# Performance work log

Measured on AMD Instinct MI355X. Metric: run time of the kernel, lower is better.

## Reference

```python
import jax, jax.numpy as jnp
import numpy as np

VOCAB, VEC, HID, ATT, DOM, B, S = 50000, 300, 256, 500, 16, 64, 128


def _gru_scan(gi_all, h0, Whh, bhh):
    # gi_all: [S,B,3H] precomputed input projections; returns hs: [S,B,H]
    def step(h, gi):
        gh = h @ Whh.T + bhh
        i_r, i_z, i_n = jnp.split(gi, 3, axis=-1)
        h_r, h_z, h_n = jnp.split(gh, 3, axis=-1)
        r = jax.nn.sigmoid(i_r + h_r)
        zg = jax.nn.sigmoid(i_z + h_z)
        n = jnp.tanh(i_n + r * h_n)
        h_new = (1.0 - zg) * n + zg * h
        return h_new, h_new
    _, hs = jax.lax.scan(step, h0, gi_all)
    return hs


def setup_inputs() -> dict:
    key = jax.random.key(0)
    ks = jax.random.split(key, 16)
    def xavier(k, shape):
        fan_in, fan_out = shape[-1], shape[0]
        std = float(np.sqrt(2.0 / (fan_in + fan_out)))
        return jax.random.normal(k, shape, dtype=jnp.float32) * std
    inp = {
        'x': jax.random.randint(ks[0], (B, S), 0, VOCAB),
        'z': jax.random.randint(ks[1], (B,), 0, DOM),
        'emb': jax.random.normal(ks[2], (VOCAB, VEC), dtype=jnp.float32) * 0.1,
        'Wih_f': xavier(ks[3], (3 * HID, VEC)),
        'Whh_f': xavier(ks[4], (3 * HID, HID)),
        'bih_f': jnp.zeros((3 * HID,), jnp.float32),
        'bhh_f': jnp.zeros((3 * HID,), jnp.float32),
        'Wih_b': xavier(ks[5], (3 * HID, VEC)),
        'Whh_b': xavier(ks[6], (3 * HID, HID)),
        'bih_b': jnp.zeros((3 * HID,), jnp.float32),
        'bhh_b': jnp.zeros((3 * HID,), jnp.float32),
        'att_fc_W': xavier(ks[7], (ATT, 2 * HID)),
        'att_fc_b': jnp.zeros((ATT,), jnp.float32),
        'att_weight': xavier(ks[8], (DOM, ATT)),
        'fc_W': xavier(ks[9], (2, 2 * HID)),
        'fc_b': jnp.zeros((2,), jnp.float32),
    }
    return inp


def reference(x, z, emb, Wih_f, Whh_f, bih_f, bhh_f, Wih_b, Whh_b, bih_b, bhh_b,
              att_fc_W, att_fc_b, att_weight, fc_W, fc_b):
    xe = emb[x]                              # [B,S,VEC]
    xs = jnp.transpose(xe, (1, 0, 2))        # [S,B,VEC] (seq-major like torch GRU)
    h0 = jnp.zeros((x.shape[0], HID), jnp.float32)
    gi_f = jnp.einsum('sbv,gv->sbg', xs, Wih_f) + bih_f
    hs_f = _gru_scan(gi_f, h0, Whh_f, bhh_f)                       # [S,B,H]
    gi_b = jnp.einsum('sbv,gv->sbg', xs[::-1], Wih_b) + bih_b
    hs_b = _gru_scan(gi_b, h0, Whh_b, bhh_b)[::-1]                 # [S,B,H]
    h = jnp.transpose(jnp.concatenate([hs_f, hs_b], axis=-1), (1, 0, 2))  # [B,S,2H]
    hr = jnp.tanh(jnp.einsum('bsh,ah->bsa', h, att_fc_W) + att_fc_b)      # [B,S,ATT]
    # batched gather of per-domain attention vector, then per-row dot
    u = jnp.einsum('bsa,ba->bs', hr, att_weight[z])                        # [B,S]
    att = jax.nn.softmax(u, axis=1)                                        # [B,S]
    pooled = jnp.einsum('bsh,bs->bh', h, att)                              # [B,2H]
    # dropout is identity in eval mode
    return pooled @ fc_W.T + fc_b                                          # [B,2]
```

## Files before the change

kernel.cpp:

```cpp
#include <hip/hip_runtime.h>
#include <math.h>

#define VEC   300
#define HID   256
#define ATT   500
#define NB    64
#define NS    128
#define G3    768
#define GIC   1536
#define H2    512

typedef _Float16 half1;
typedef _Float16 h2_t  __attribute__((ext_vector_type(2)));
typedef _Float16 f16x8 __attribute__((ext_vector_type(8)));
typedef float    f32x4 __attribute__((ext_vector_type(4)));

struct __align__(16) H8 { h2_t a, b, c, d; };

#if __has_builtin(__builtin_amdgcn_exp2f)
#define EXP2F(x) __builtin_amdgcn_exp2f(x)
#else
#define EXP2F(x) exp2f(x)
#endif
#if __has_builtin(__builtin_amdgcn_rcpf)
#define RCPF(x) __builtin_amdgcn_rcpf(x)
#else
#define RCPF(x) (1.0f/(x))
#endif

__device__ __forceinline__ float sigm(float x){ return RCPF(1.f + EXP2F(-1.44269504f*x)); }
__device__ __forceinline__ float tanh_fast(float x){ return 1.f - 2.f*RCPF(1.f + EXP2F(2.88539008f*x)); }

#if __has_builtin(__builtin_amdgcn_fdot2)
#define FDOT(w,h,acc) __builtin_amdgcn_fdot2((w),(h),(acc),false)
#else
#define FDOT(w,h,acc) ((acc) + (float)(w).x*(float)(h).x + (float)(w).y*(float)(h).y)
#endif

__global__ __launch_bounds__(256) void k_prep2(const float* __restrict__ Wf,
                       const float* __restrict__ Wb, h2_t* __restrict__ Wpk){
  int o = blockIdx.x*256 + threadIdx.x;
  int t = o & 511;
  int rest = o >> 9;
  int j = rest % 3;
  int p = (rest/3) & 63;
  int dir = rest / 192;
  int u = (t >> 6)*32 + (t & 31);
  int ks = (t >> 5) & 1;
  const float* W = dir ? Wb : Wf;
  int k0 = ks*128 + 2*p;
  h2_t w;
  w.x = (half1)W[(j*HID+u)*HID + k0];
  w.y = (half1)W[(j*HID+u)*HID + k0 + 1];
  Wpk[o] = w;
}

__global__ __launch_bounds__(256) void k_prepA(const float* __restrict__ afW,
                       half1* __restrict__ afW16){
  int o = blockIdx.x*256 + threadIdx.x;
  int n = o >> 9, k = o & 511;
  afW16[o] = (half1)((n < ATT) ? afW[n*H2 + k] : 0.f);
}

__global__ __launch_bounds__(256)
__attribute__((amdgpu_waves_per_eu(4, 4)))
void k_gi_mfma(const int* __restrict__ x,
      const float* __restrict__ emb,
      const float* __restrict__ Wf, const float* __restrict__ Wb,
      const float* __restrict__ bf, const float* __restrict__ bb,
      float* __restrict__ gi){
  __shared__ half1 Al[128*40];
  __shared__ half1 Bl[128*40];
  __shared__ int   xi[128];
  const int t = threadIdx.x;
  const int row0 = blockIdx.x * 128;
  const int col0 = blockIdx.y * 128;
  if (t < 128) {
    int i = row0 + t; int s = i >> 6; int b = i & 63;
    xi[t] = x[b*NS + s];
  }
  __syncthreads();

  const int lane = t & 63, wid = t >> 6;
  const int wr = wid >> 1, wc = wid & 1;
  const int l15 = lane & 15, lk = lane >> 4;

  f32x4 acc[4][4];
#pragma unroll
  for (int i = 0; i < 4; ++i)
#pragma unroll
    for (int j = 0; j < 4; ++j) acc[i][j] = (f32x4){0.f,0.f,0.f,0.f};

  for (int ks = 0; ks < 10; ++ks) {
#pragma unroll
    for (int l = 0; l < 8; ++l) {
      int idx = l*256 + t;
      int row = idx >> 4;
      int kp  = idx & 15;
      int kk  = ks*32 + kp*2;
      h2_t va; va.x = (half1)0.f; va.y = (half1)0.f;
      h2_t vb; vb.x = (half1)0.f; vb.y = (half1)0.f;
      if (kk < VEC) {
        float2 e = *reinterpret_cast<const float2*>(&emb[(long)xi[row]*VEC + kk]);
        va.x = (half1)e.x; va.y = (half1)e.y;
        int g = col0 + row;
        const float* W = (g < G3) ? &Wf[(long)g*VEC] : &Wb[(long)(g-G3)*VEC];
        float2 w2 = *reinterpret_cast<const float2*>(&W[kk]);
        vb.x = (half1)w2.x; vb.y = (half1)w2.y;
      }
      *reinterpret_cast<h2_t*>(&Al[row*40 + kp*2]) = va;
      *reinterpret_cast<h2_t*>(&Bl[row*40 + kp*2]) = vb;
    }
    __syncthreads();
    f16x8 af[4], bfq[4];
#pragma unroll
    for (int i = 0; i < 4; ++i)
      af[i]  = *reinterpret_cast<const f16x8*>(&Al[(wr*64 + i*16 + l15)*40 + lk*8]);
#pragma unroll
    for (int j = 0; j < 4; ++j)
      bfq[j] = *reinterpret_cast<const f16x8*>(&Bl[(wc*64 + j*16 + l15)*40 + lk*8]);
#pragma unroll
    for (int i = 0; i < 4; ++i)
#pragma unroll
      for (int j = 0; j < 4; ++j)
        acc[i][j] = __builtin_amdgcn_mfma_f32_16x16x32_f16(af[i], bfq[j], acc[i][j], 0, 0, 0);
    __syncthreads();
  }

#pragma unroll
  for (int j = 0; j < 4; ++j) {
    int gcol = col0 + wc*64 + j*16 + l15;
    float bj = (gcol < G3) ? bf[gcol] : bb[gcol - G3];
#pragma unroll
    for (int i = 0; i < 4; ++i) {
      int grow0 = row0 + wr*64 + i*16 + lk*4;
#pragma unroll
      for (int q = 0; q < 4; ++q)
        gi[(long)(grow0 + q)*GIC + gcol] = acc[i][j][q] + bj;
    }
  }
}

#define DECL12(X,g,UNUSED) h2_t X##g##a0,X##g##a1,X##g##a2, X##g##b0,X##g##b1,X##g##b2, \
                                X##g##c0,X##g##c1,X##g##c2, X##g##d0,X##g##d1,X##g##d2;
#define LOAD12(X,g,PB) \
  X##g##a0=wp[(((PB)+4*(g)+0)*3+0)*512]; X##g##a1=wp[(((PB)+4*(g)+0)*3+1)*512]; X##g##a2=wp[(((PB)+4*(g)+0)*3+2)*512]; \
  X##g##b0=wp[(((PB)+4*(g)+1)*3+0)*512]; X##g##b1=wp[(((PB)+4*(g)+1)*3+1)*512]; X##g##b2=wp[(((PB)+4*(g)+1)*3+2)*512]; \
  X##g##c0=wp[(((PB)+4*(g)+2)*3+0)*512]; X##g##c1=wp[(((PB)+4*(g)+2)*3+1)*512]; X##g##c2=wp[(((PB)+4*(g)+2)*3+2)*512]; \
  X##g##d0=wp[(((PB)+4*(g)+3)*3+0)*512]; X##g##d1=wp[(((PB)+4*(g)+3)*3+1)*512]; X##g##d2=wp[(((PB)+4*(g)+3)*3+2)*512];
#define FMA12(X,g,BOFF) { \
  H8 hv = *reinterpret_cast<const H8*>(&hr[(BOFF) + (g)*8]); \
  a0=FDOT(X##g##a0,hv.a,a0); a1=FDOT(X##g##a1,hv.a,a1); a2=FDOT(X##g##a2,hv.a,a2); \
  a0=FDOT(X##g##b0,hv.b,a0); a1=FDOT(X##g##b1,hv.b,a1); a2=FDOT(X##g##b2,hv.b,a2); \
  a0=FDOT(X##g##c0,hv.c,a0); a1=FDOT(X##g##c1,hv.c,a1); a2=FDOT(X##g##c2,hv.c,a2); \
  a0=FDOT(X##g##d0,hv.d,a0); a1=FDOT(X##g##d1,hv.d,a1); a2=FDOT(X##g##d2,hv.d,a2); }
#define GRP8(M,X,A2) M(X,0,A2) M(X,1,A2) M(X,2,A2) M(X,3,A2) M(X,4,A2) M(X,5,A2) M(X,6,A2) M(X,7,A2)

__global__ __launch_bounds__(512)
__attribute__((amdgpu_waves_per_eu(2, 2)))
void k_scan_reg6(const float* __restrict__ gi,
     const h2_t* __restrict__ Wpk,
     const float* __restrict__ bhf, const float* __restrict__ bhb,
     float* __restrict__ hseq){
  __shared__ __align__(16) half1 hist[129*256];
  const int t    = threadIdx.x;
  const int lane = t & 63;
  const int ul   = lane & 31;
  const int ks   = lane >> 5;
  const int w    = t >> 6;
  const int u    = w*32 + ul;
  const int ks128 = ks * 128;
  const int dir  = blockIdx.x & 1;
  const int b    = blockIdx.x >> 1;
  const float* bhh = dir ? bhb : bhf;
  const h2_t* wp = Wpk + (long)dir*98304 + t;

  GRP8(DECL12, A, 0)
  GRP8(DECL12, B, 0)
  GRP8(LOAD12, A, 0)
  GRP8(LOAD12, B, 32)

  const bool fin = (ks == 0);
  float bh0=0.f, bh1=0.f, bh2=0.f;
  if (fin) { bh0 = bhh[u]; bh1 = bhh[HID+u]; bh2 = bhh[2*HID+u]; }
  if (t < 256) hist[t] = (half1)0.f;
  float hprev = 0.f;

  const long gstep = dir ? -(long)NB*GIC : (long)NB*GIC;
  long gbase = ((long)(dir ? (NS-1) : 0)*NB + b)*GIC + dir*G3 + u;
  __syncthreads();

#pragma unroll 1
  for (int tt = 0; tt < NS; ++tt) {
    float i0=0.f, i1=0.f, i2=0.f;
    if (fin) {
      i0 = gi[gbase]; i1 = gi[gbase+HID]; i2 = gi[gbase+2*HID];
    }
    const half1* hr = &hist[tt*256 + ks128];
    float a0=0.f, a1=0.f, a2=0.f;
    GRP8(FMA12, A, 0)
    GRP8(FMA12, B, 64)
    a0 += __shfl_xor(a0, 32, 64);
    a1 += __shfl_xor(a1, 32, 64);
    a2 += __shfl_xor(a2, 32, 64);
    if (fin) {
      float g0 = bh0 + a0;
      float g1 = bh1 + a1;
      float g2 = bh2 + a2;
      float r  = sigm(i0 + g0);
      float zg = sigm(i1 + g1);
      float n  = tanh_fast(i2 + r*g2);
      float hn = (1.f - zg)*n + zg*hprev;
      hprev = hn;
      hist[(tt+1)*256 + u] = (half1)hn;
    }
    gbase += gstep;
    __syncthreads();
  }

#pragma unroll 1
  for (int it = 0; it < 16; ++it) {
    int idx = it*512 + t;
    int ttr = idx >> 6;
    int c4  = (idx & 63) * 4;
    int s   = dir ? (NS-1-ttr) : ttr;
    h2_t p0 = *reinterpret_cast<const h2_t*>(&hist[(ttr+1)*256 + c4]);
    h2_t p1 = *reinterpret_cast<const h2_t*>(&hist[(ttr+1)*256 + c4 + 2]);
    float4 v; v.x = (float)p0.x; v.y = (float)p0.y; v.z = (float)p1.x; v.w = (float)p1.y;
    *reinterpret_cast<float4*>(&hseq[((long)b*NS + s)*H2 + dir*HID + c4]) = v;
  }
}

__global__ __launch_bounds__(256)
__attribute__((amdgpu_waves_per_eu(4, 4)))
void k_att1_mfma(const float* __restrict__ hseq, const half1* __restrict__ afW16,
    const float* __restrict__ afb, const float* __restrict__ attw,
    const int* __restrict__ z, float* __restrict__ ub){
  __shared__ half1 Ah[32*520];
  __shared__ float red[4*32];
  const int t  = threadIdx.x;
  const int b  = blockIdx.x;
  const int s0 = blockIdx.y * 32;
  const int lane = t & 63, w = t >> 6;
  const int l15 = lane & 15, lk = lane >> 4;

#pragma unroll
  for (int l = 0; l < 64; ++l) {
    int idx = l*256 + t;
    int sl = idx >> 9, c = idx & 511;
    Ah[sl*520 + c] = (half1)hseq[((long)b*NS + s0 + sl)*H2 + c];
  }
  __syncthreads();

  f32x4 acc[2][8];
#pragma unroll
  for (int i = 0; i < 2; ++i)
#pragma unroll
    for (int j = 0; j < 8; ++j) acc[i][j] = (f32x4){0.f,0.f,0.f,0.f};

#pragma unroll 2
  for (int ksn = 0; ksn < 16; ++ksn) {
    f16x8 af[2];
#pragma unroll
    for (int mt = 0; mt < 2; ++mt)
      af[mt] = *reinterpret_cast<const f16x8*>(&Ah[(mt*16 + l15)*520 + ksn*32 + lk*8]);
#pragma unroll
    for (int nt = 0; nt < 8; ++nt) {
      int n = w*128 + nt*16 + l15;
      f16x8 bf = *reinterpret_cast<const f16x8*>(&afW16[(long)n*512 + ksn*32 + lk*8]);
#pragma unroll
      for (int mt = 0; mt < 2; ++mt)
        acc[mt][nt] = __builtin_amdgcn_mfma_f32_16x16x32_f16(af[mt], bf, acc[mt][nt], 0, 0, 0);
    }
  }

  float us[8];
#pragma unroll
  for (int i = 0; i < 8; ++i) us[i] = 0.f;
  const int zb = z[b];
#pragma unroll
  for (int nt = 0; nt < 8; ++nt) {
    int n = w*128 + nt*16 + l15;
    float ab = (n < ATT) ? afb[n] : 0.f;
    float aw = (n < ATT) ? attw[zb*ATT + n] : 0.f;
#pragma unroll
    for (int mt = 0; mt < 2; ++mt)
#pragma unroll
      for (int q = 0; q < 4; ++q)
        us[mt*4+q] += tanh_fast(acc[mt][nt][q] + ab) * aw;
  }
#pragma unroll
  for (int off = 1; off < 16; off <<= 1)
#pragma unroll
    for (int i = 0; i < 8; ++i) us[i] += __shfl_xor(us[i], off, 64);
  if (l15 == 0) {
#pragma unroll
    for (int i = 0; i < 8; ++i) {
      int row = (i >> 2)*16 + lk*4 + (i & 3);
      red[w*32 + row] = us[i];
    }
  }
  __syncthreads();
  if (t < 32)
    ub[b*NS + s0 + t] = red[t] + red[32+t] + red[64+t] + red[96+t];
}

__global__ __launch_bounds__(256) void k_att2(const float* __restrict__ hseq,
   const float* __restrict__ ub, const float* __restrict__ fcW,
   const float* __restrict__ fcb, float* __restrict__ out){
  __shared__ float att[NS];
  __shared__ float red[256];
  __shared__ float pool[H2];
  const int t = threadIdx.x, b = blockIdx.x;
  float v = (t < NS) ? ub[b*NS + t] : -3.4e38f;
  red[t] = v; __syncthreads();
  for (int off = 128; off >= 1; off >>= 1) {
    if (t < off) red[t] = fmaxf(red[t], red[t+off]);
    __syncthreads();
  }
  float mx = red[0]; __syncthreads();
  float e = (t < NS) ? EXP2F(1.44269504f*(v - mx)) : 0.f;
  red[t] = e; __syncthreads();
  for (int off = 128; off >= 1; off >>= 1) {
    if (t < off) red[t] += red[t+off];
    __syncthreads();
  }
  float sm = red[0]; __syncthreads();
  if (t < NS) att[t] = e / sm;
  __syncthreads();
#pragma unroll
  for (int rep = 0; rep < 2; ++rep) {
    int c = rep*256 + t;
    float acc = 0.f;
#pragma unroll 4
    for (int s = 0; s < NS; ++s) acc += att[s] * hseq[((long)b*NS + s)*H2 + c];
    pool[c] = acc;
  }
  __syncthreads();
  for (int j = 0; j < 2; ++j) {
    float p = pool[t]*fcW[j*H2+t] + pool[t+256]*fcW[j*H2+t+256];
    red[t] = p; __syncthreads();
    for (int off = 128; off >= 1; off >>= 1) {
      if (t < off) red[t] += red[t+off];
      __syncthreads();
    }
    if (t == 0) out[b*2+j] = red[0] + fcb[j];
    __syncthreads();
  }
}

extern "C" void kernel_launch(void* const* d_in, const int* in_sizes, int n_in,
                              void* d_out, int out_size, void* d_ws, size_t ws_size,
                              hipStream_t stream) {
  const int*   x     = (const int*)  d_in[0];
  const int*   z     = (const int*)  d_in[1];
  const float* emb   = (const float*)d_in[2];
  const float* Wih_f = (const float*)d_in[3];
  const float* Whh_f = (const float*)d_in[4];
  const float* bih_f = (const float*)d_in[5];
  const float* bhh_f = (const float*)d_in[6];
  const float* Wih_b = (const float*)d_in[7];
  const float* Whh_b = (const float*)d_in[8];
  const float* bih_b = (const float*)d_in[9];
  const float* bhh_b = (const float*)d_in[10];
  const float* afW   = (const float*)d_in[11];
  const float* afb   = (const float*)d_in[12];
  const float* attw  = (const float*)d_in[13];
  const float* fcW   = (const float*)d_in[14];
  const float* fcb   = (const float*)d_in[15];

  float* ws    = (float*)d_ws;
  h2_t*  Wpk   = (h2_t*)ws;
  half1* afW16 = (half1*)(ws + 196608);
  float* giW   = ws   + 196608 + 131072;
  float* hseq  = giW  + 12582912;
  float* ubuf  = hseq + 4194304;

  k_prep2<<<dim3(768),  dim3(256), 0, stream>>>(Whh_f, Whh_b, Wpk);
  k_prepA<<<dim3(1024), dim3(256), 0, stream>>>(afW, afW16);
  k_gi_mfma<<<dim3(64,12), dim3(256), 0, stream>>>(x, emb, Wih_f, Wih_b, bih_f, bih_b, giW);
  k_scan_reg6<<<dim3(128), dim3(512), 0, stream>>>(giW, Wpk, bhh_f, bhh_b, hseq);
  k_att1_mfma<<<dim3(64,4), dim3(256), 0, stream>>>(hseq, afW16, afb, attw, z, ubuf);
  k_att2<<<dim3(64), dim3(256), 0, stream>>>(hseq, ubuf, fcW, fcb, (float*)d_out);
}
```

Measured before the change: 233.7 us.

## Pre-pack embeddings and input weights to fp16, store gate inputs in fp16

Adds a prep kernel that gathers the embeddings and converts them plus the input-projection weights to padded fp16 buffers. The projection GEMM then loads MFMA fragments straight from global memory with no LDS staging or barriers. The gate-input tensor is written and read by the scan in fp16, halving its memory traffic. The cost is an extra kernel launch and a materialized fp16 embedding buffer, plus lower precision on the gate inputs.

```diff
diff --git a/kernel.cpp b/kernel.cpp
--- a/kernel.cpp
+++ b/kernel.cpp
@@ -9,6 +9,7 @@
 #define G3    768
 #define GIC   1536
 #define H2    512
+#define KP    320
 
 typedef _Float16 half1;
 typedef _Float16 h2_t  __attribute__((ext_vector_type(2)));
@@ -62,25 +63,46 @@
   afW16[o] = (half1)((n < ATT) ? afW[n*H2 + k] : 0.f);
 }
 
+__global__ __launch_bounds__(256) void k_prepXW(const int* __restrict__ x,
+      const float* __restrict__ emb,
+      const float* __restrict__ Wf, const float* __restrict__ Wb,
+      h2_t* __restrict__ xe16, h2_t* __restrict__ W16){
+  int o = blockIdx.x*256 + threadIdx.x;
+  const int NXE = 8192*160;
+  if (o < NXE) {
+    int i = o / 160, kp = o - 160*(o/160);
+    int k0 = kp*2;
+    int s = i >> 6, b = i & 63;
+    h2_t v; v.x = (half1)0.f; v.y = (half1)0.f;
+    if (k0 < VEC) {
+      const float* e = &emb[(long)x[b*NS + s]*VEC];
+      v.x = (half1)e[k0];
+      v.y = (half1)((k0+1 < VEC) ? e[k0+1] : 0.f);
+    }
+    xe16[(long)i*160 + kp] = v;
+  } else {
+    int o2 = o - NXE;
+    if (o2 >= 1536*160) return;
+    int g = o2 / 160, kp = o2 - 160*(o2/160);
+    int k0 = kp*2;
+    h2_t v; v.x = (half1)0.f; v.y = (half1)0.f;
+    if (k0 < VEC) {
+      const float* wr = (g < G3) ? &Wf[(long)g*VEC] : &Wb[(long)(g-G3)*VEC];
+      v.x = (half1)wr[k0];
+      v.y = (half1)((k0+1 < VEC) ? wr[k0+1] : 0.f);
+    }
+    W16[(long)g*160 + kp] = v;
+  }
+}
+
 __global__ __launch_bounds__(256)
 __attribute__((amdgpu_waves_per_eu(4, 4)))
-void k_gi_mfma(const int* __restrict__ x,
-      const float* __restrict__ emb,
-      const float* __restrict__ Wf, const float* __restrict__ Wb,
+void k_gi16(const half1* __restrict__ xe16, const half1* __restrict__ W16,
       const float* __restrict__ bf, const float* __restrict__ bb,
-      float* __restrict__ gi){
-  __shared__ half1 Al[128*40];
-  __shared__ half1 Bl[128*40];
-  __shared__ int   xi[128];
+      half1* __restrict__ gi16){
   const int t = threadIdx.x;
   const int row0 = blockIdx.x * 128;
   const int col0 = blockIdx.y * 128;
-  if (t < 128) {
-    int i = row0 + t; int s = i >> 6; int b = i & 63;
-    xi[t] = x[b*NS + s];
-  }
-  __syncthreads();
-
   const int lane = t & 63, wid = t >> 6;
   const int wr = wid >> 1, wc = wid & 1;
   const int l15 = lane & 15, lk = lane >> 4;
@@ -91,40 +113,24 @@
 #pragma unroll
     for (int j = 0; j < 4; ++j) acc[i][j] = (f32x4){0.f,0.f,0.f,0.f};
 
+#pragma unroll 1
   for (int ks = 0; ks < 10; ++ks) {
-#pragma unroll
-    for (int l = 0; l < 8; ++l) {
-      int idx = l*256 + t;
-      int row = idx >> 4;
-      int kp  = idx & 15;
-      int kk  = ks*32 + kp*2;
-      h2_t va; va.x = (half1)0.f; va.y = (half1)0.f;
-      h2_t vb; vb.x = (half1)0.f; vb.y = (half1)0.f;
-      if (kk < VEC) {
-        float2 e = *reinterpret_cast<const float2*>(&emb[(long)xi[row]*VEC + kk]);
-        va.x = (half1)e.x; va.y = (half1)e.y;
-        int g = col0 + row;
-        const float* W = (g < G3) ? &Wf[(long)g*VEC] : &Wb[(long)(g-G3)*VEC];
-        float2 w2 = *reinterpret_cast<const float2*>(&W[kk]);
-        vb.x = (half1)w2.x; vb.y = (half1)w2.y;
-      }
-      *reinterpret_cast<h2_t*>(&Al[row*40 + kp*2]) = va;
-      *reinterpret_cast<h2_t*>(&Bl[row*40 + kp*2]) = vb;
-    }
-    __syncthreads();
     f16x8 af[4], bfq[4];
 #pragma unroll
-    for (int i = 0; i < 4; ++i)
-      af[i]  = *reinterpret_cast<const f16x8*>(&Al[(wr*64 + i*16 + l15)*40 + lk*8]);
-#pragma unroll
-    for (int j = 0; j < 4; ++j)
-      bfq[j] = *reinterpret_cast<const f16x8*>(&Bl[(wc*64 + j*16 + l15)*40 + lk*8]);
+    for (int i = 0; i < 4; ++i) {
+      int row = row0 + wr*64 + i*16 + l15;
+      af[i] = *reinterpret_cast<const f16x8*>(&xe16[(long)row*KP + ks*32 + lk*8]);
+    }
+#pragma unroll
+    for (int j = 0; j < 4; ++j) {
+      int g = col0 + wc*64 + j*16 + l15;
+      bfq[j] = *reinterpret_cast<const f16x8*>(&W16[(long)g*KP + ks*32 + lk*8]);
+    }
 #pragma unroll
     for (int i = 0; i < 4; ++i)
 #pragma unroll
       for (int j = 0; j < 4; ++j)
         acc[i][j] = __builtin_amdgcn_mfma_f32_16x16x32_f16(af[i], bfq[j], acc[i][j], 0, 0, 0);
-    __syncthreads();
   }
 
 #pragma unroll
@@ -136,7 +142,7 @@
       int grow0 = row0 + wr*64 + i*16 + lk*4;
 #pragma unroll
       for (int q = 0; q < 4; ++q)
-        gi[(long)(grow0 + q)*GIC + gcol] = acc[i][j][q] + bj;
+        gi16[(long)(grow0 + q)*GIC + gcol] = (half1)(acc[i][j][q] + bj);
     }
   }
 }
@@ -158,7 +164,7 @@
 
 __global__ __launch_bounds__(512)
 __attribute__((amdgpu_waves_per_eu(2, 2)))
-void k_scan_reg6(const float* __restrict__ gi,
+void k_scan_reg8(const half1* __restrict__ gi16,
      const h2_t* __restrict__ Wpk,
      const float* __restrict__ bhf, const float* __restrict__ bhb,
      float* __restrict__ hseq){
@@ -194,7 +200,9 @@
   for (int tt = 0; tt < NS; ++tt) {
     float i0=0.f, i1=0.f, i2=0.f;
     if (fin) {
-      i0 = gi[gbase]; i1 = gi[gbase+HID]; i2 = gi[gbase+2*HID];
+      i0 = (float)gi16[gbase];
+      i1 = (float)gi16[gbase+HID];
+      i2 = (float)gi16[gbase+2*HID];
     }
     const half1* hr = &hist[tt*256 + ks128];
     float a0=0.f, a1=0.f, a2=0.f;
@@ -372,14 +380,18 @@
   float* ws    = (float*)d_ws;
   h2_t*  Wpk   = (h2_t*)ws;
   half1* afW16 = (half1*)(ws + 196608);
-  float* giW   = ws   + 196608 + 131072;
-  float* hseq  = giW  + 12582912;
+  h2_t*  xe16  = (h2_t*)(ws + 196608 + 131072);
+  h2_t*  W16   = (h2_t*)(ws + 196608 + 131072 + 1310720);
+  half1* gi16  = (half1*)(ws + 196608 + 131072 + 1310720 + 245760);
+  float* hseq  = ws + 196608 + 131072 + 1310720 + 245760 + 6291456;
   float* ubuf  = hseq + 4194304;
 
-  k_prep2<<<dim3(768),  dim3(256), 0, stream>>>(Whh_f, Whh_b, Wpk);
-  k_prepA<<<dim3(1024), dim3(256), 0, stream>>>(afW, afW16);
-  k_gi_mfma<<<dim3(64,12), dim3(256), 0, stream>>>(x, emb, Wih_f, Wih_b, bih_f, bih_b, giW);
-  k_scan_reg6<<<dim3(128), dim3(512), 0, stream>>>(giW, Wpk, bhh_f, bhh_b, hseq);
+  k_prep2 <<<dim3(768),  dim3(256), 0, stream>>>(Whh_f, Whh_b, Wpk);
+  k_prepA <<<dim3(1024), dim3(256), 0, stream>>>(afW, afW16);
+  k_prepXW<<<dim3(6080), dim3(256), 0, stream>>>(x, emb, Wih_f, Wih_b, xe16, W16);
+  k_gi16  <<<dim3(64,12), dim3(256), 0, stream>>>((const half1*)xe16, (const half1*)W16,
+                                                  bih_f, bih_b, gi16);
+  k_scan_reg8<<<dim3(128), dim3(512), 0, stream>>>(gi16, Wpk, bhh_f, bhh_b, hseq);
   k_att1_mfma<<<dim3(64,4), dim3(256), 0, stream>>>(hseq, afW16, afb, attw, z, ubuf);
   k_att2<<<dim3(64), dim3(256), 0, stream>>>(hseq, ubuf, fcW, fcb, (float*)d_out);
 }
```

Result: slower. 268.4 us (+14.8%).
